# Performance work log

Measured on AMD Instinct MI355X. Metric: run time of the kernel, lower is better.

## Reference

```python
import jax, jax.numpy as jnp
import numpy as np

T = 2048        # packed token count (q_len)
HID = 2560      # hidden_size
H = 40          # num_heads
NOPE = 64       # qk_nope_head_dim
ROPE = 32       # qk_rope_head_dim
V = 64          # v_head_dim
QLORA = 768     # q_lora_rank
KVLORA = 256    # kv_lora_rank
EPS = 1e-5
THETA = 10000.0


def setup_inputs() -> dict:
    key = jax.random.key(0)
    ks = jax.random.split(key, 8)
    s = 0.02
    return {
        "positions": jnp.arange(T, dtype=jnp.int32),
        "hidden_states": jax.random.normal(ks[0], (T, HID), jnp.float32),
        "w_qa": jax.random.normal(ks[1], (HID, QLORA), jnp.float32) * s,
        "g_qa": jnp.ones((QLORA,), jnp.float32),
        "w_qb": jax.random.normal(ks[2], (QLORA, H * (NOPE + ROPE)), jnp.float32) * s,
        "w_kva": jax.random.normal(ks[3], (HID, KVLORA + ROPE), jnp.float32) * s,
        "g_kva": jnp.ones((KVLORA,), jnp.float32),
        "w_kc": jax.random.normal(ks[4], (H, NOPE, KVLORA), jnp.float32) * s,  # absorbed K weight
        "w_vc": jax.random.normal(ks[5], (H, KVLORA, V), jnp.float32) * s,     # absorbed V weight
        "w_o": jax.random.normal(ks[6], (H * V, HID), jnp.float32) * s,
    }


def _rms(x, g):
    return x * jax.lax.rsqrt(jnp.mean(x * x, axis=-1, keepdims=True) + EPS) * g


def _rope_rotate(x, cos, sin):
    # NeoX-style rotary: rotate halves of the last (ROPE) dim.
    half = ROPE // 2
    x1, x2 = x[..., :half], x[..., half:]
    return jnp.concatenate([x1 * cos - x2 * sin, x2 * cos + x1 * sin], axis=-1)


def reference(positions, hidden_states, w_qa, g_qa, w_qb, w_kva, g_kva, w_kc, w_vc, w_o):
    # Low-rank Q path: q_a_proj -> RMSNorm -> q_b_proj
    q = _rms(hidden_states @ w_qa, g_qa) @ w_qb                       # [T, H*(NOPE+ROPE)]
    q = q.reshape(T, H, NOPE + ROPE)
    q_nope, q_pe = q[..., :NOPE], q[..., NOPE:]

    # Weight absorption: project q_nope into latent space (bmm with w_kc)
    q_lat = jnp.einsum('thn,hnk->thk', q_nope, w_kc)                  # [T, H, KVLORA]

    # Compressed KV path (single shared latent head)
    latent = hidden_states @ w_kva                                    # [T, KVLORA+ROPE]
    v_in = _rms(latent[:, :KVLORA], g_kva)                            # [T, KVLORA]
    k_pe = latent[:, KVLORA:]                                         # [T, ROPE]

    # Partial-head RoPE on the rope slices
    half = ROPE // 2
    inv_freq = 1.0 / (THETA ** (jnp.arange(half, dtype=jnp.float32) / half))
    f = positions.astype(jnp.float32)[:, None] * inv_freq             # [T, half]
    cos, sin = jnp.cos(f), jnp.sin(f)
    q_pe = _rope_rotate(q_pe, cos[:, None, :], sin[:, None, :])       # [T, H, ROPE]
    k_pe = _rope_rotate(k_pe, cos, sin)                               # [T, ROPE]

    # Packed q/k feeding the latent-cache attention (MQA, head_dim = KVLORA+ROPE)
    q_in = jnp.concatenate([q_lat, q_pe], axis=-1)                    # [T, H, 288]
    k_in = jnp.concatenate([v_in, k_pe], axis=-1)                     # [T, 288]

    scale = (NOPE + ROPE) ** -0.5
    scores = jnp.einsum('thd,sd->hts', q_in, k_in) * scale            # [H, T, T]
    causal = jnp.tril(jnp.ones((T, T), dtype=bool))
    scores = jnp.where(causal, scores, -jnp.inf)
    probs = jax.nn.softmax(scores, axis=-1)
    o_lat = jnp.einsum('hts,sk->thk', probs, v_in)                    # [T, H, KVLORA]

    # Un-absorb: bmm with w_vc, then output projection
    o = jnp.einsum('thk,hkv->thv', o_lat, w_vc).reshape(T, H * V)     # [T, H*V]
    return o @ w_o                                                    # [T, HID]
```

## Files before the change

kernel.cpp:

```cpp
#include <hip/hip_runtime.h>
#include <hip/hip_bf16.h>
#include <math.h>

#define TT 2048
#define HID 2560
#define NH 40
#define NOPE 64
#define ROPE 32
#define VDIM 64
#define QLORA 768
#define KVLORA 256
#define DQK 288
#define QHD 96
#define EPS 1e-5f
#define THETA 10000.0f

typedef __attribute__((ext_vector_type(8))) short bf16x8;
typedef __attribute__((ext_vector_type(4))) float f32x4;
typedef __attribute__((address_space(1))) const void* gas_t;
typedef __attribute__((address_space(3))) void* las_t;

static __device__ __forceinline__ ushort f2bf(float x) {
    __hip_bfloat16 b = __float2bfloat16(x);
    return *reinterpret_cast<ushort*>(&b);
}

__global__ __launch_bounds__(256) void cast_bf16(const float* __restrict__ x,
                                                 ushort* __restrict__ y, int n) {
    int i = (blockIdx.x * 256 + threadIdx.x) * 4;
    if (i + 3 < n) {
        float4 v = *(const float4*)(x + i);
        y[i]     = f2bf(v.x);
        y[i + 1] = f2bf(v.y);
        y[i + 2] = f2bf(v.z);
        y[i + 3] = f2bf(v.w);
    }
}

__global__ __launch_bounds__(256) void transpose_cast(const float* __restrict__ w,
                                                      ushort* __restrict__ wt,
                                                      int K, int N) {
    __shared__ float tile[32][33];
    int bn = blockIdx.x * 32, bk = blockIdx.y * 32;
    int tx = threadIdx.x % 32, ty = threadIdx.x / 32;
    #pragma unroll
    for (int i = 0; i < 32; i += 8) {
        int k = bk + ty + i, n = bn + tx;
        if (k < K && n < N) tile[ty + i][tx] = w[(size_t)k * N + n];
    }
    __syncthreads();
    #pragma unroll
    for (int i = 0; i < 32; i += 8) {
        int n = bn + ty + i, k = bk + tx;
        if (n < N && k < K) wt[(size_t)n * K + k] = f2bf(tile[tx][ty + i]);
    }
}

__global__ __launch_bounds__(256, 2) void gemm_bf16(const ushort* __restrict__ A,
                                                    const ushort* __restrict__ Bt,
                                                    float* __restrict__ C,
                                                    int M, int N, int K) {
    __shared__ ushort As[128 * 32];
    __shared__ ushort Bs[128 * 32];
    const int tid  = threadIdx.x;
    const int lane = tid & 63;
    const int wv   = tid >> 6;
    const int col  = lane & 15;
    const int quad = lane >> 4;
    const int m0 = blockIdx.y * 128, n0 = blockIdx.x * 128;
    const int wr = (wv >> 1) * 64, wc = (wv & 1) * 64;

    f32x4 acc[4][4];
    #pragma unroll
    for (int i = 0; i < 4; i++)
        #pragma unroll
        for (int j = 0; j < 4; j++) acc[i][j] = (f32x4){0.f, 0.f, 0.f, 0.f};

    for (int k0 = 0; k0 < K; k0 += 32) {
        #pragma unroll
        for (int j = 0; j < 2; j++) {
            int slot = wv * 128 + j * 64 + lane;
            int row  = slot >> 2;
            int ch   = slot & 3;
            const ushort* ga = A + (size_t)(m0 + row) * K + k0 + ch * 8;
            __builtin_amdgcn_global_load_lds((gas_t)ga, (las_t)(As + slot * 8), 16, 0, 0);
            int brow = n0 + row; if (brow >= N) brow = N - 1;
            const ushort* gb = Bt + (size_t)brow * K + k0 + ch * 8;
            __builtin_amdgcn_global_load_lds((gas_t)gb, (las_t)(Bs + slot * 8), 16, 0, 0);
        }
        __syncthreads();
        bf16x8 af[4], bfr[4];
        #pragma unroll
        for (int i = 0; i < 4; i++)
            af[i] = *(const bf16x8*)(As + (wr + i * 16 + col) * 32 + quad * 8);
        #pragma unroll
        for (int j = 0; j < 4; j++)
            bfr[j] = *(const bf16x8*)(Bs + (wc + j * 16 + col) * 32 + quad * 8);
        #pragma unroll
        for (int i = 0; i < 4; i++)
            #pragma unroll
            for (int j = 0; j < 4; j++)
                acc[i][j] = __builtin_amdgcn_mfma_f32_16x16x32_bf16(af[i], bfr[j], acc[i][j], 0, 0, 0);
        __syncthreads();
    }
    #pragma unroll
    for (int i = 0; i < 4; i++) {
        int gr = m0 + wr + i * 16 + quad * 4;
        #pragma unroll
        for (int j = 0; j < 4; j++) {
            int gc = n0 + wc + j * 16 + col;
            if (gc < N) {
                #pragma unroll
                for (int r = 0; r < 4; r++)
                    C[(size_t)(gr + r) * N + gc] = acc[i][j][r];
            }
        }
    }
}

__global__ __launch_bounds__(256, 4) void gemm_bf16_n64(const ushort* __restrict__ A,
                                                        const ushort* __restrict__ Bt,
                                                        float* __restrict__ C,
                                                        int M, int N, int K) {
    __shared__ ushort As[128 * 32];
    __shared__ ushort Bs[64 * 32];
    const int tid  = threadIdx.x;
    const int lane = tid & 63;
    const int wv   = tid >> 6;
    const int col  = lane & 15;
    const int quad = lane >> 4;
    const int m0 = blockIdx.y * 128, n0 = blockIdx.x * 64;
    const int wr = wv * 32;

    f32x4 acc[2][4];
    #pragma unroll
    for (int i = 0; i < 2; i++)
        #pragma unroll
        for (int j = 0; j < 4; j++) acc[i][j] = (f32x4){0.f, 0.f, 0.f, 0.f};

    for (int k0 = 0; k0 < K; k0 += 32) {
        #pragma unroll
        for (int j = 0; j < 2; j++) {
            int slot = j * 256 + tid;
            int row  = slot >> 2;
            int ch   = slot & 3;
            const ushort* ga = A + (size_t)(m0 + row) * K + k0 + ch * 8;
            __builtin_amdgcn_global_load_lds((gas_t)ga, (las_t)(As + slot * 8), 16, 0, 0);
        }
        {
            int row = tid >> 2;
            int ch  = tid & 3;
            int brow = n0 + row; if (brow >= N) brow = N - 1;
            const ushort* gb = Bt + (size_t)brow * K + k0 + ch * 8;
            __builtin_amdgcn_global_load_lds((gas_t)gb, (las_t)(Bs + tid * 8), 16, 0, 0);
        }
        __syncthreads();
        bf16x8 af[2], bfr[4];
        #pragma unroll
        for (int i = 0; i < 2; i++)
            af[i] = *(const bf16x8*)(As + (wr + i * 16 + col) * 32 + quad * 8);
        #pragma unroll
        for (int j = 0; j < 4; j++)
            bfr[j] = *(const bf16x8*)(Bs + (j * 16 + col) * 32 + quad * 8);
        #pragma unroll
        for (int i = 0; i < 2; i++)
            #pragma unroll
            for (int j = 0; j < 4; j++)
                acc[i][j] = __builtin_amdgcn_mfma_f32_16x16x32_bf16(af[i], bfr[j], acc[i][j], 0, 0, 0);
        __syncthreads();
    }
    #pragma unroll
    for (int i = 0; i < 2; i++) {
        int gr = m0 + wr + i * 16 + quad * 4;
        #pragma unroll
        for (int j = 0; j < 4; j++) {
            int gc = n0 + j * 16 + col;
            if (gc < N) {
                #pragma unroll
                for (int r = 0; r < 4; r++)
                    C[(size_t)(gr + r) * N + gc] = acc[i][j][r];
            }
        }
    }
}

__global__ __launch_bounds__(256) void rms_qa(const float* __restrict__ x,
                                              const float* __restrict__ g,
                                              ushort* __restrict__ y) {
    int t = blockIdx.x, tid = threadIdx.x;
    __shared__ float red[256];
    __shared__ float s_inv;
    const float* row = x + (size_t)t * QLORA;
    float ss = 0.f;
    for (int i = tid; i < QLORA; i += 256) { float v = row[i]; ss += v * v; }
    red[tid] = ss; __syncthreads();
    for (int s = 128; s > 0; s >>= 1) { if (tid < s) red[tid] += red[tid + s]; __syncthreads(); }
    if (tid == 0) s_inv = rsqrtf(red[0] / (float)QLORA + EPS);
    __syncthreads();
    float si = s_inv;
    ushort* orow = y + (size_t)t * QLORA;
    for (int i = tid; i < QLORA; i += 256) orow[i] = f2bf(row[i] * si * g[i]);
}

__global__ __launch_bounds__(256) void kin_post(const float* __restrict__ kin,
                                                const float* __restrict__ g,
                                                const int* __restrict__ positions,
                                                ushort* __restrict__ kin_bf) {
    int t = blockIdx.x, tid = threadIdx.x;
    __shared__ float red[256];
    __shared__ float s_inv;
    const float* row = kin + (size_t)t * DQK;
    float v = row[tid];
    red[tid] = v * v; __syncthreads();
    for (int s = 128; s > 0; s >>= 1) { if (tid < s) red[tid] += red[tid + s]; __syncthreads(); }
    if (tid == 0) s_inv = rsqrtf(red[0] / (float)KVLORA + EPS);
    __syncthreads();
    ushort* orow = kin_bf + (size_t)t * DQK;
    orow[tid] = f2bf(v * s_inv * g[tid]);
    if (tid < 16) {
        float pos = (float)positions[t];
        float freq = powf(THETA, -(float)tid / 16.0f);
        float f = pos * freq;
        float c = cosf(f), s = sinf(f);
        float x1 = row[KVLORA + tid], x2 = row[KVLORA + 16 + tid];
        orow[KVLORA + tid]      = f2bf(x1 * c - x2 * s);
        orow[KVLORA + 16 + tid] = f2bf(x2 * c + x1 * s);
    }
}

#define QTB 16
__global__ __launch_bounds__(256) void build_qin(const float* __restrict__ q,
                                                 const float* __restrict__ w_kc,
                                                 const int* __restrict__ positions,
                                                 ushort* __restrict__ qin) {
    int tb = blockIdx.x * QTB, h = blockIdx.y, tid = threadIdx.x;
    const float scale = 0.10206207261596577f;
    __shared__ float qn[QTB][NOPE];
    __shared__ float qp[QTB][ROPE];
    for (int i = tid; i < QTB * QHD; i += 256) {
        int r = i / QHD, cidx = i % QHD;
        float v = q[(size_t)(tb + r) * (NH * QHD) + h * QHD + cidx];
        if (cidx < NOPE) qn[r][cidx] = v;
        else             qp[r][cidx - NOPE] = v;
    }
    __syncthreads();
    int k = tid;
    float acc[QTB];
    #pragma unroll
    for (int r = 0; r < QTB; r++) acc[r] = 0.f;
    const float* w = w_kc + (size_t)h * NOPE * KVLORA + k;
    for (int n = 0; n < NOPE; n++) {
        float wval = w[(size_t)n * KVLORA];
        #pragma unroll
        for (int r = 0; r < QTB; r++) acc[r] += qn[r][n] * wval;
    }
    #pragma unroll
    for (int r = 0; r < QTB; r++)
        qin[((size_t)(tb + r) * NH + h) * DQK + k] = f2bf(acc[r] * scale);
    int r = tid >> 4, fi = tid & 15;
    float pos = (float)positions[tb + r];
    float freq = powf(THETA, -(float)fi / 16.0f);
    float f = pos * freq;
    float c = cosf(f), s = sinf(f);
    float x1 = qp[r][fi], x2 = qp[r][16 + fi];
    ushort* orow = qin + ((size_t)(tb + r) * NH + h) * DQK;
    orow[KVLORA + fi]      = f2bf((x1 * c - x2 * s) * scale);
    orow[KVLORA + 16 + fi] = f2bf((x2 * c + x1 * s) * scale);
}

#define KSTR 296
#define VSTR 72
#define PSTR 72

__global__ __launch_bounds__(256, 2) void flash_attn(const ushort* __restrict__ qin,
                                                     const ushort* __restrict__ kin,
                                                     float* __restrict__ o_lat) {
    __shared__ ushort lds[64 * KSTR + 256 * VSTR];
    ushort* krow = lds;
    ushort* vt   = lds + 64 * KSTR;
    ushort* pbuf = lds;

    const int tid  = threadIdx.x;
    const int lane = tid & 63;
    const int wv   = tid >> 6;
    const int col  = lane & 15;
    const int quad = lane >> 4;
    const int h    = blockIdx.y;
    const int qb   = ((int)gridDim.x - 1 - (int)blockIdx.x) * 64;

    bf16x8 qf[9];
    {
        const ushort* base = qin + ((size_t)(qb + wv * 16 + col) * NH + h) * DQK + quad * 8;
        #pragma unroll
        for (int k = 0; k < 9; k++) qf[k] = *(const bf16x8*)(base + k * 32);
    }

    f32x4 of[16];
    #pragma unroll
    for (int i = 0; i < 16; i++) of[i] = (f32x4){0.f, 0.f, 0.f, 0.f};
    float m_i[4] = {-1e30f, -1e30f, -1e30f, -1e30f};
    float l_i[4] = {0.f, 0.f, 0.f, 0.f};

    for (int s0 = 0; s0 <= qb; s0 += 64) {
        __syncthreads();
        {
            const ushort* src = kin + (size_t)(s0 + lane) * DQK;
            #pragma unroll
            for (int ci = 0; ci < 9; ci++) {
                int c = ci * 4 + wv;
                uint4 u = *(const uint4*)(src + c * 8);
                *(uint4*)(krow + lane * KSTR + c * 8) = u;
                if (c < 32) {
                    const ushort* up = (const ushort*)&u;
                    #pragma unroll
                    for (int j = 0; j < 8; j++)
                        vt[(c * 8 + j) * VSTR + lane] = up[j];
                }
            }
        }
        __syncthreads();
        f32x4 sf[4];
        #pragma unroll
        for (int tc = 0; tc < 4; tc++) sf[tc] = (f32x4){0.f, 0.f, 0.f, 0.f};
        #pragma unroll
        for (int k = 0; k < 9; k++) {
            #pragma unroll
            for (int tc = 0; tc < 4; tc++) {
                bf16x8 bf = *(const bf16x8*)(krow + (tc * 16 + col) * KSTR + k * 32 + quad * 8);
                sf[tc] = __builtin_amdgcn_mfma_f32_16x16x32_bf16(qf[k], bf, sf[tc], 0, 0, 0);
            }
        }
        if (s0 == qb) {
            #pragma unroll
            for (int tc = 0; tc < 4; tc++)
                #pragma unroll
                for (int r = 0; r < 4; r++)
                    if (tc * 16 + col > wv * 16 + quad * 4 + r) sf[tc][r] = -1e30f;
        }
        float mnew[4], alpha[4];
        #pragma unroll
        for (int r = 0; r < 4; r++) {
            float mx = fmaxf(fmaxf(sf[0][r], sf[1][r]), fmaxf(sf[2][r], sf[3][r]));
            mx = fmaxf(mx, __shfl_xor(mx, 1));
            mx = fmaxf(mx, __shfl_xor(mx, 2));
            mx = fmaxf(mx, __shfl_xor(mx, 4));
            mx = fmaxf(mx, __shfl_xor(mx, 8));
            mnew[r] = fmaxf(m_i[r], mx);
            alpha[r] = __expf(m_i[r] - mnew[r]);
            m_i[r] = mnew[r];
        }
        float rsum[4];
        #pragma unroll
        for (int r = 0; r < 4; r++) {
            float s = 0.f;
            #pragma unroll
            for (int tc = 0; tc < 4; tc++) {
                float p = __expf(sf[tc][r] - mnew[r]);
                sf[tc][r] = p;
                s += p;
            }
            s += __shfl_xor(s, 1);
            s += __shfl_xor(s, 2);
            s += __shfl_xor(s, 4);
            s += __shfl_xor(s, 8);
            rsum[r] = s;
        }
        #pragma unroll
        for (int r = 0; r < 4; r++) l_i[r] = l_i[r] * alpha[r] + rsum[r];
        #pragma unroll
        for (int i = 0; i < 16; i++)
            #pragma unroll
            for (int r = 0; r < 4; r++) of[i][r] *= alpha[r];
        __syncthreads();
        #pragma unroll
        for (int tc = 0; tc < 4; tc++)
            #pragma unroll
            for (int r = 0; r < 4; r++)
                pbuf[(wv * 16 + quad * 4 + r) * PSTR + tc * 16 + col] = f2bf(sf[tc][r]);
        __syncthreads();
        bf16x8 pa[2];
        #pragma unroll
        for (int ks = 0; ks < 2; ks++)
            pa[ks] = *(const bf16x8*)(pbuf + (wv * 16 + col) * PSTR + ks * 32 + quad * 8);
        #pragma unroll
        for (int nt = 0; nt < 16; nt++) {
            #pragma unroll
            for (int ks = 0; ks < 2; ks++) {
                bf16x8 vb = *(const bf16x8*)(vt + (nt * 16 + col) * VSTR + ks * 32 + quad * 8);
                of[nt] = __builtin_amdgcn_mfma_f32_16x16x32_bf16(pa[ks], vb, of[nt], 0, 0, 0);
            }
        }
    }
    #pragma unroll
    for (int r = 0; r < 4; r++) {
        float inv = 1.0f / l_i[r];
        int row = qb + wv * 16 + quad * 4 + r;
        float* dst = o_lat + ((size_t)row * NH + h) * KVLORA + col;
        #pragma unroll
        for (int nt = 0; nt < 16; nt++) dst[nt * 16] = of[nt][r] * inv;
    }
}

__global__ __launch_bounds__(256) void ogemm(const float* __restrict__ o_lat,
                                             const float* __restrict__ w_vc,
                                             ushort* __restrict__ o) {
    int tb = blockIdx.x * 16, h = blockIdx.y, tid = threadIdx.x;
    __shared__ float ol[16][KVLORA];
    for (int i = tid; i < 16 * KVLORA; i += 256) {
        int r = i >> 8, k = i & 255;
        ol[r][k] = o_lat[((size_t)(tb + r) * NH + h) * KVLORA + k];
    }
    __syncthreads();
    int v = tid & 63, r0 = tid >> 6;
    float acc[4] = {0.f, 0.f, 0.f, 0.f};
    const float* w = w_vc + (size_t)h * KVLORA * VDIM + v;
    for (int k = 0; k < KVLORA; k++) {
        float wval = w[(size_t)k * VDIM];
        #pragma unroll
        for (int j = 0; j < 4; j++) acc[j] += ol[r0 + j * 4][k] * wval;
    }
    #pragma unroll
    for (int j = 0; j < 4; j++)
        o[(size_t)(tb + r0 + j * 4) * HID + h * VDIM + v] = f2bf(acc[j]);
}

extern "C" void kernel_launch(void* const* d_in, const int* in_sizes, int n_in,
                              void* d_out, int out_size, void* d_ws, size_t ws_size,
                              hipStream_t stream) {
    const int*   positions = (const int*)d_in[0];
    const float* hs    = (const float*)d_in[1];
    const float* w_qa  = (const float*)d_in[2];
    const float* g_qa  = (const float*)d_in[3];
    const float* w_qb  = (const float*)d_in[4];
    const float* w_kva = (const float*)d_in[5];
    const float* g_kva = (const float*)d_in[6];
    const float* w_kc  = (const float*)d_in[7];
    const float* w_vc  = (const float*)d_in[8];
    const float* w_o   = (const float*)d_in[9];
    float* out = (float*)d_out;

    float* ws    = (float*)d_ws;
    float* qa    = ws;
    float* q     = qa    + (size_t)TT * QLORA;
    float* kin   = q     + (size_t)TT * NH * QHD;
    float* o_lat = kin   + (size_t)TT * DQK;
    ushort* ub     = (ushort*)(o_lat + (size_t)TT * NH * KVLORA);
    ushort* hs_bf  = ub;
    ushort* qa_bf  = hs_bf  + (size_t)TT * HID;
    ushort* o_bf   = qa_bf  + (size_t)TT * QLORA;
    ushort* kin_bf = o_bf   + (size_t)TT * HID;
    ushort* qin_bf = kin_bf + (size_t)TT * DQK;
    ushort* w_qa_t  = qin_bf + (size_t)TT * NH * DQK;
    ushort* w_qb_t  = w_qa_t + (size_t)QLORA * HID;
    ushort* w_kva_t = w_qb_t + (size_t)(NH * QHD) * QLORA;
    ushort* w_o_t   = w_kva_t + (size_t)DQK * HID;

    cast_bf16<<<(TT * HID) / 1024, 256, 0, stream>>>(hs, hs_bf, TT * HID);
    transpose_cast<<<dim3(QLORA / 32, HID / 32), 256, 0, stream>>>(w_qa, w_qa_t, HID, QLORA);
    transpose_cast<<<dim3((NH * QHD) / 32, QLORA / 32), 256, 0, stream>>>(w_qb, w_qb_t, QLORA, NH * QHD);
    transpose_cast<<<dim3(DQK / 32, HID / 32), 256, 0, stream>>>(w_kva, w_kva_t, HID, DQK);
    transpose_cast<<<dim3(HID / 32, HID / 32), 256, 0, stream>>>(w_o, w_o_t, HID, HID);

    gemm_bf16_n64<<<dim3(QLORA / 64, TT / 128), 256, 0, stream>>>(hs_bf, w_qa_t, qa, TT, QLORA, HID);
    rms_qa<<<TT, 256, 0, stream>>>(qa, g_qa, qa_bf);
    gemm_bf16<<<dim3((NH * QHD) / 128, TT / 128), 256, 0, stream>>>(qa_bf, w_qb_t, q, TT, NH * QHD, QLORA);
    gemm_bf16_n64<<<dim3((DQK + 63) / 64, TT / 128), 256, 0, stream>>>(hs_bf, w_kva_t, kin, TT, DQK, HID);
    kin_post<<<TT, 256, 0, stream>>>(kin, g_kva, positions, kin_bf);
    build_qin<<<dim3(TT / QTB, NH), 256, 0, stream>>>(q, w_kc, positions, qin_bf);
    flash_attn<<<dim3(TT / 64, NH), 256, 0, stream>>>(qin_bf, kin_bf, o_lat);
    ogemm<<<dim3(TT / 16, NH), 256, 0, stream>>>(o_lat, w_vc, o_bf);
    gemm_bf16<<<dim3(HID / 128, TT / 128), 256, 0, stream>>>(o_bf, w_o_t, out, TT, HID, HID);
}
```

Baseline: 839.2 us.

## Fuse w_vc un-absorb projection into flash attention epilogue using MFMA

The flash attention kernel now normalizes its latent output, stages it as bf16 in LDS together with a pre-transposed bf16 w_vc slice, and runs the per-head 256->64 projection with MFMA instructions before writing o_bf directly. This removes the fp32 o_lat round trip through global memory (about 84 MB written and read back) and the scalar-FMA ogemm kernel. A new transpose kernel converts w_vc to bf16 each call. The intermediate o_lat is now rounded to bf16, and the epilogue adds LDS use and a sync at the end of attention.

New measurement: 778.8 us. -7.2%, faster.

```diff
diff --git a/kernel.cpp b/kernel.cpp
--- a/kernel.cpp
+++ b/kernel.cpp
@@ -54,6 +54,23 @@
         int n = bn + ty + i, k = bk + tx;
         if (n < N && k < K) wt[(size_t)n * K + k] = f2bf(tile[tx][ty + i]);
     }
+}
+
+__global__ __launch_bounds__(256) void transpose_vc(const float* __restrict__ w,
+                                                    ushort* __restrict__ wt) {
+    __shared__ float tile[32][33];
+    int h = blockIdx.z;
+    const float* src = w + (size_t)h * KVLORA * VDIM;
+    ushort* dst = wt + (size_t)h * VDIM * KVLORA;
+    int bn = blockIdx.x * 32, bk = blockIdx.y * 32;
+    int tx = threadIdx.x % 32, ty = threadIdx.x / 32;
+    #pragma unroll
+    for (int i = 0; i < 32; i += 8)
+        tile[ty + i][tx] = src[(size_t)(bk + ty + i) * VDIM + bn + tx];
+    __syncthreads();
+    #pragma unroll
+    for (int i = 0; i < 32; i += 8)
+        dst[(size_t)(bn + ty + i) * KVLORA + bk + tx] = f2bf(tile[tx][ty + i]);
 }
 
 __global__ __launch_bounds__(256, 2) void gemm_bf16(const ushort* __restrict__ A,
@@ -271,11 +288,13 @@
 #define KSTR 296
 #define VSTR 72
 #define PSTR 72
+#define OSTR 264
 
 __global__ __launch_bounds__(256, 2) void flash_attn(const ushort* __restrict__ qin,
                                                      const ushort* __restrict__ kin,
-                                                     float* __restrict__ o_lat) {
-    __shared__ ushort lds[64 * KSTR + 256 * VSTR];
+                                                     const ushort* __restrict__ w_vct,
+                                                     ushort* __restrict__ o_bf) {
+    __shared__ __align__(16) ushort lds[64 * KSTR + 256 * VSTR];
     ushort* krow = lds;
     ushort* vt   = lds + 64 * KSTR;
     ushort* pbuf = lds;
@@ -391,37 +410,47 @@
             }
         }
     }
-    #pragma unroll
-    for (int r = 0; r < 4; r++) {
-        float inv = 1.0f / l_i[r];
-        int row = qb + wv * 16 + quad * 4 + r;
-        float* dst = o_lat + ((size_t)row * NH + h) * KVLORA + col;
-        #pragma unroll
-        for (int nt = 0; nt < 16; nt++) dst[nt * 16] = of[nt][r] * inv;
-    }
-}
-
-__global__ __launch_bounds__(256) void ogemm(const float* __restrict__ o_lat,
-                                             const float* __restrict__ w_vc,
-                                             ushort* __restrict__ o) {
-    int tb = blockIdx.x * 16, h = blockIdx.y, tid = threadIdx.x;
-    __shared__ float ol[16][KVLORA];
-    for (int i = tid; i < 16 * KVLORA; i += 256) {
-        int r = i >> 8, k = i & 255;
-        ol[r][k] = o_lat[((size_t)(tb + r) * NH + h) * KVLORA + k];
-    }
-    __syncthreads();
-    int v = tid & 63, r0 = tid >> 6;
-    float acc[4] = {0.f, 0.f, 0.f, 0.f};
-    const float* w = w_vc + (size_t)h * KVLORA * VDIM + v;
-    for (int k = 0; k < KVLORA; k++) {
-        float wval = w[(size_t)k * VDIM];
-        #pragma unroll
-        for (int j = 0; j < 4; j++) acc[j] += ol[r0 + j * 4][k] * wval;
-    }
-    #pragma unroll
-    for (int j = 0; j < 4; j++)
-        o[(size_t)(tb + r0 + j * 4) * HID + h * VDIM + v] = f2bf(acc[j]);
+
+    __syncthreads();
+    ushort* obuf = lds;
+    ushort* wbuf = lds + 64 * KSTR;
+    {
+        float inv_l[4];
+        #pragma unroll
+        for (int r = 0; r < 4; r++) inv_l[r] = 1.0f / l_i[r];
+        #pragma unroll
+        for (int nt = 0; nt < 16; nt++)
+            #pragma unroll
+            for (int r = 0; r < 4; r++)
+                obuf[(wv * 16 + quad * 4 + r) * OSTR + nt * 16 + col] = f2bf(of[nt][r] * inv_l[r]);
+        const ushort* wsrc = w_vct + (size_t)h * VDIM * KVLORA;
+        #pragma unroll
+        for (int i = 0; i < 8; i++) {
+            int s = i * 256 + tid;
+            int row = s >> 5, ch = s & 31;
+            *(uint4*)(wbuf + row * OSTR + ch * 8) = *(const uint4*)(wsrc + (size_t)row * KVLORA + ch * 8);
+        }
+    }
+    __syncthreads();
+    f32x4 acc[4];
+    #pragma unroll
+    for (int j = 0; j < 4; j++) acc[j] = (f32x4){0.f, 0.f, 0.f, 0.f};
+    #pragma unroll
+    for (int ks = 0; ks < 8; ks++) {
+        bf16x8 af = *(const bf16x8*)(obuf + (wv * 16 + col) * OSTR + ks * 32 + quad * 8);
+        #pragma unroll
+        for (int j = 0; j < 4; j++) {
+            bf16x8 bw = *(const bf16x8*)(wbuf + (j * 16 + col) * OSTR + ks * 32 + quad * 8);
+            acc[j] = __builtin_amdgcn_mfma_f32_16x16x32_bf16(af, bw, acc[j], 0, 0, 0);
+        }
+    }
+    #pragma unroll
+    for (int j = 0; j < 4; j++) {
+        int gc = h * VDIM + j * 16 + col;
+        #pragma unroll
+        for (int r = 0; r < 4; r++)
+            o_bf[(size_t)(qb + wv * 16 + quad * 4 + r) * HID + gc] = f2bf(acc[j][r]);
+    }
 }
 
 extern "C" void kernel_launch(void* const* d_in, const int* in_sizes, int n_in,
@@ -443,8 +472,7 @@
     float* qa    = ws;
     float* q     = qa    + (size_t)TT * QLORA;
     float* kin   = q     + (size_t)TT * NH * QHD;
-    float* o_lat = kin   + (size_t)TT * DQK;
-    ushort* ub     = (ushort*)(o_lat + (size_t)TT * NH * KVLORA);
+    ushort* ub     = (ushort*)(kin + (size_t)TT * DQK);
     ushort* hs_bf  = ub;
     ushort* qa_bf  = hs_bf  + (size_t)TT * HID;
     ushort* o_bf   = qa_bf  + (size_t)TT * QLORA;
@@ -454,12 +482,14 @@
     ushort* w_qb_t  = w_qa_t + (size_t)QLORA * HID;
     ushort* w_kva_t = w_qb_t + (size_t)(NH * QHD) * QLORA;
     ushort* w_o_t   = w_kva_t + (size_t)DQK * HID;
+    ushort* w_vc_t  = w_o_t + (size_t)HID * HID;
 
     cast_bf16<<<(TT * HID) / 1024, 256, 0, stream>>>(hs, hs_bf, TT * HID);
     transpose_cast<<<dim3(QLORA / 32, HID / 32), 256, 0, stream>>>(w_qa, w_qa_t, HID, QLORA);
     transpose_cast<<<dim3((NH * QHD) / 32, QLORA / 32), 256, 0, stream>>>(w_qb, w_qb_t, QLORA, NH * QHD);
     transpose_cast<<<dim3(DQK / 32, HID / 32), 256, 0, stream>>>(w_kva, w_kva_t, HID, DQK);
     transpose_cast<<<dim3(HID / 32, HID / 32), 256, 0, stream>>>(w_o, w_o_t, HID, HID);
+    transpose_vc<<<dim3(VDIM / 32, KVLORA / 32, NH), 256, 0, stream>>>(w_vc, w_vc_t);
 
     gemm_bf16_n64<<<dim3(QLORA / 64, TT / 128), 256, 0, stream>>>(hs_bf, w_qa_t, qa, TT, QLORA, HID);
     rms_qa<<<TT, 256, 0, stream>>>(qa, g_qa, qa_bf);
@@ -467,7 +497,6 @@
     gemm_bf16_n64<<<dim3((DQK + 63) / 64, TT / 128), 256, 0, stream>>>(hs_bf, w_kva_t, kin, TT, DQK, HID);
     kin_post<<<TT, 256, 0, stream>>>(kin, g_kva, positions, kin_bf);
     build_qin<<<dim3(TT / QTB, NH), 256, 0, stream>>>(q, w_kc, positions, qin_bf);
-    flash_attn<<<dim3(TT / 64, NH), 256, 0, stream>>>(qin_bf, kin_bf, o_lat);
-    ogemm<<<dim3(TT / 16, NH), 256, 0, stream>>>(o_lat, w_vc, o_bf);
+    flash_attn<<<dim3(TT / 64, NH), 256, 0, stream>>>(qin_bf, kin_bf, w_vc_t, o_bf);
     gemm_bf16<<<dim3(HID / 128, TT / 128), 256, 0, stream>>>(o_bf, w_o_t, out, TT, HID, HID);
 }
```
